# Kernel tuning notes

Measured on AMD Instinct MI355X. Metric: run time of the kernel, lower is better.

The kernel has to match this reference:

```python
import jax, jax.numpy as jnp
import numpy as np

N, E, D, H = 50000, 600000, 128, 256
EPS_DENOM = 1e-7   # epsilon added to sigmoid-edge denominator in the torch code
EPS_NORM = 1e-5    # InstanceNorm1d default eps


def _fcnn(x, Wa, ba, Wb, bb):
    # FCNN: Linear -> ReLU -> Linear
    return jax.nn.relu(x @ Wa + ba) @ Wb + bb


def setup_inputs() -> dict:
    key = jax.random.key(0)
    ks = jax.random.split(key, 16)
    inp = {
        "node_features": jax.random.normal(ks[0], (1, N, D), jnp.float32),
        "edge_index": jax.random.randint(ks[1], (1, 2, E), 0, N, dtype=jnp.int64)
        if jax.config.jax_enable_x64 else jax.random.randint(ks[1], (1, 2, E), 0, N, dtype=jnp.int32),
        "edge_features": jax.random.normal(ks[2], (1, E, D), jnp.float32),
        "global_features": jax.random.normal(ks[3], (1, 1, D), jnp.float32),
    }
    # three FCNNs: fc1 (D->H), fc2 (H->D), Kaiming-uniform-ish init scale 1/sqrt(fan_in)
    names = ["W1a", "b1a", "W1b", "b1b", "W2a", "b2a", "W2b", "b2b", "W3a", "b3a", "W3b", "b3b"]
    shapes = [(D, H), (H,), (H, D), (D,)] * 3
    fans = [D, D, H, H] * 3
    for k, (nm, sh, fan) in zip(ks[4:], zip(names, shapes, fans)):
        bound = 1.0 / np.sqrt(fan)
        inp[nm] = jax.random.uniform(k, sh, jnp.float32, -bound, bound)
    return inp


def reference(node_features, edge_index, edge_features, global_features,
              W1a, b1a, W1b, b1b, W2a, b2a, W2b, b2b, W3a, b3a, W3b, b3b):
    x = node_features[0]                      # [N, D]
    src = edge_index[0, 0]                    # [E]
    dst = edge_index[0, 1]                    # [E]
    s = jax.nn.sigmoid(edge_features[0])      # [E, D]

    # denominator: eps + sum of sigmoid(edge_feat) over all edges incident to node i
    denom = (EPS_DENOM
             + jax.ops.segment_sum(s, src, num_segments=N)
             + jax.ops.segment_sum(s, dst, num_segments=N))   # [N, D]

    h1 = _fcnn(x, W1a, b1a, W1b, b1b)                          # [N, D] self term
    h2 = _fcnn(x, W2a, b2a, W2b, b2b)                          # [N, D] neighbor term
    g3 = _fcnn(global_features[0, 0], W3a, b3a, W3b, b3b)      # [D]    global term

    # sum over incident edges of sigmoid(e) * FCNN_two(x_neighbor), then / denom
    agg = (jax.ops.segment_sum(s * h2[dst], src, num_segments=N)
           + jax.ops.segment_sum(s * h2[src], dst, num_segments=N))  # [N, D]

    inter = h1 + agg / denom + g3                              # [N, D]

    # InstanceNorm1d on a (1, D) vector: normalize over the feature dim (no affine)
    mu = jnp.mean(inter, axis=-1, keepdims=True)
    var = jnp.var(inter, axis=-1, keepdims=True)
    normed = (inter - mu) / jnp.sqrt(var + EPS_NORM)
    # dropout(p=0.1) treated as identity (inference mode)

    out = x + jax.nn.relu(normed)                              # residual update
    return out[None]                                           # [1, N, D]
```

## Files before the change

kernel.cpp:

```cpp
#include <hip/hip_runtime.h>
#include <math.h>

#define DD 128
#define HH 256

typedef __attribute__((ext_vector_type(8))) short bf16x8;
typedef __attribute__((ext_vector_type(4))) float f32x4;
typedef __attribute__((ext_vector_type(2))) float f32x2;
typedef unsigned short u16;
typedef unsigned int u32;
typedef unsigned char u8;

__device__ __forceinline__ float bf2f(u16 u) {
  union { u32 i; float f; } v; v.i = ((u32)u) << 16; return v.f;
}
__device__ __forceinline__ u16 f2bf(float f) {
  union { u32 i; float f; } v; v.f = f;
  u32 r = v.i + 0x7FFFu + ((v.i >> 16) & 1u);
  return (u16)(r >> 16);
}

#define GA_T 512
#define GA_C 512
__global__ __launch_bounds__(256) void mergeA(
    const float* __restrict__ W1a, const float* __restrict__ W1b,
    const float* __restrict__ W2a, const float* __restrict__ W2b,
    u16* __restrict__ o1, u16* __restrict__ o2,
    u16* __restrict__ o3, u16* __restrict__ o4,
    const float* __restrict__ gf,
    const float* __restrict__ W3a, const float* __restrict__ b3a,
    const float* __restrict__ W3b, const float* __restrict__ b3b,
    float* __restrict__ g3out,
    const int* __restrict__ eix, u32* __restrict__ deg, int twoE) {
  const int b = blockIdx.x;
  if (b < GA_T) {
    int idx = b * 256 + threadIdx.x;
    int m = idx >> 15;
    int r = idx & 32767;
    const float* in; u16* out; int K, Nc;
    if (m == 0)      { in = W1a; out = o1; K = DD; Nc = HH; }
    else if (m == 1) { in = W1b; out = o2; K = HH; Nc = DD; }
    else if (m == 2) { in = W2a; out = o3; K = DD; Nc = HH; }
    else             { in = W2b; out = o4; K = HH; Nc = DD; }
    int k = r / Nc, n = r % Nc;
    out[n * K + k] = f2bf(in[r]);
  } else if (b == GA_T) {
    __shared__ float gs[DD];
    __shared__ float hs[HH];
    int t = threadIdx.x;
    if (t < DD) gs[t] = gf[t];
    __syncthreads();
    float acc = b3a[t];
    for (int k = 0; k < DD; ++k) acc = fmaf(gs[k], W3a[k * HH + t], acc);
    hs[t] = acc > 0.f ? acc : 0.f;
    __syncthreads();
    if (t < DD) {
      float o = b3b[t];
      for (int j = 0; j < HH; ++j) o = fmaf(hs[j], W3b[j * DD + t], o);
      g3out[t] = o;
    }
  } else {
    int t = (b - GA_T - 1) * 256 + threadIdx.x;
    const int stride = GA_C * 256;
    for (; t < twoE; t += stride) atomicAdd(&deg[eix[t]], 1u);
  }
}

__global__ __launch_bounds__(1024) void scan_kernel(const u32* __restrict__ deg,
    u32* __restrict__ rowstart, u32* __restrict__ cursor, int N) {
  __shared__ u32 wsum[16];
  const int t = threadIdx.x;
  const int w = t >> 6, lane = t & 63;
  const int span = ((N + 1023) & ~1023) >> 4;
  const int b = w * span;
  const int e = min(b + span, N);

  u32 s = 0;
  for (int i = b + lane; i < e; i += 64) s += deg[i];
#pragma unroll
  for (int off = 32; off; off >>= 1) s += __shfl_xor(s, off);
  if (lane == 0) wsum[w] = s;
  __syncthreads();

  u32 carry = 0;
  for (int i = 0; i < w; ++i) carry += wsum[i];

  for (int i0 = b; i0 < e; i0 += 64) {
    int i = i0 + lane;
    u32 v = (i < e) ? deg[i] : 0u;
    u32 inc = v;
#pragma unroll
    for (int off = 1; off < 64; off <<= 1) {
      u32 u2 = __shfl_up(inc, off);
      if (lane >= off) inc += u2;
    }
    u32 excl = carry + inc - v;
    if (i < e) { rowstart[i] = excl; cursor[i] = excl; }
    carry += __shfl(inc, 63);
  }
  if (w == 15 && lane == 63) rowstart[N] = carry;
}

__global__ __launch_bounds__(256) void gemm_l1(const float* __restrict__ x,
    const u16* __restrict__ w1aT, const float* __restrict__ b1a,
    const u16* __restrict__ w2aT, const float* __restrict__ b2a,
    u16* __restrict__ hid, int M) {
  const int wave = (blockIdx.x * 256 + threadIdx.x) >> 6;
  const int lane = threadIdx.x & 63;
  const int totalWaves = (gridDim.x * 256) >> 6;
  const int nc = wave & 7;
  const int mw = wave >> 3;
  const int mStride = totalWaves >> 3;
  const int which = nc >> 2;
  const int c0 = (nc & 3) * 64;
  const u16* wT = which ? w2aT : w1aT;
  const float* bs = which ? b2a : b1a;
  const int l15 = lane & 15, l4 = lane >> 4;

  bf16x8 bfrag[4][4];
  float bcol[4];
#pragma unroll
  for (int t = 0; t < 4; ++t) {
    const int col = c0 + t * 16 + l15;
    const u16* bb = wT + (size_t)col * DD + l4 * 8;
#pragma unroll
    for (int kb = 0; kb < 4; ++kb) bfrag[kb][t] = *(const bf16x8*)(bb + kb * 32);
    bcol[t] = bs[col];
  }

  const int mTiles = (M + 15) >> 4;
  for (int mt = mw; mt < mTiles; mt += mStride) {
    const int m0 = mt << 4;
    int rowA = m0 + l15; if (rowA >= M) rowA = M - 1;
    const float* xr = x + (size_t)rowA * DD + l4 * 8;
    bf16x8 ax[4];
#pragma unroll
    for (int kb = 0; kb < 4; ++kb) {
      f32x4 a = *(const f32x4*)(xr + kb * 32);
      f32x4 b = *(const f32x4*)(xr + kb * 32 + 4);
      bf16x8 v;
      v[0] = (short)f2bf(a.x); v[1] = (short)f2bf(a.y);
      v[2] = (short)f2bf(a.z); v[3] = (short)f2bf(a.w);
      v[4] = (short)f2bf(b.x); v[5] = (short)f2bf(b.y);
      v[6] = (short)f2bf(b.z); v[7] = (short)f2bf(b.w);
      ax[kb] = v;
    }
    f32x4 acc[4] = {{0,0,0,0},{0,0,0,0},{0,0,0,0},{0,0,0,0}};
#pragma unroll
    for (int kb = 0; kb < 4; ++kb)
#pragma unroll
      for (int t = 0; t < 4; ++t)
        acc[t] = __builtin_amdgcn_mfma_f32_16x16x32_bf16(ax[kb], bfrag[kb][t], acc[t], 0, 0, 0);
#pragma unroll
    for (int t = 0; t < 4; ++t)
#pragma unroll
      for (int r = 0; r < 4; ++r) {
        const int row = m0 + l4 * 4 + r;
        float v = acc[t][r] + bcol[t];
        v = v > 0.f ? v : 0.f;
        if (row < M) hid[(size_t)row * 512 + which * 256 + c0 + t * 16 + l15] = f2bf(v);
      }
  }
}

__global__ __launch_bounds__(256) void gemm_l2(const u16* __restrict__ hid,
    const u16* __restrict__ w1bT, const float* __restrict__ b1b,
    const u16* __restrict__ w2bT, const float* __restrict__ b2b,
    u16* __restrict__ h1, u16* __restrict__ h2, int M) {
  const int wave = (blockIdx.x * 256 + threadIdx.x) >> 6;
  const int lane = threadIdx.x & 63;
  const int totalWaves = (gridDim.x * 256) >> 6;
  const int nc = wave & 3;
  const int mw = wave >> 2;
  const int mStride = totalWaves >> 2;
  const int which = nc >> 1;
  const int c0 = (nc & 1) * 64;
  const u16* wT = which ? w2bT : w1bT;
  const float* bs = which ? b2b : b1b;
  u16* Dst = which ? h2 : h1;
  const int l15 = lane & 15, l4 = lane >> 4;

  bf16x8 bfrag[8][4];
  float bcol[4];
#pragma unroll
  for (int t = 0; t < 4; ++t) {
    const int col = c0 + t * 16 + l15;
    const u16* bb = wT + (size_t)col * HH + l4 * 8;
#pragma unroll
    for (int kb = 0; kb < 8; ++kb) bfrag[kb][t] = *(const bf16x8*)(bb + kb * 32);
    bcol[t] = bs[col];
  }

  const int mTiles = (M + 15) >> 4;
  for (int mt = mw; mt < mTiles; mt += mStride) {
    const int m0 = mt << 4;
    int rowA = m0 + l15; if (rowA >= M) rowA = M - 1;
    const u16* arow = hid + (size_t)rowA * 512 + which * 256 + l4 * 8;
    f32x4 acc[4] = {{0,0,0,0},{0,0,0,0},{0,0,0,0},{0,0,0,0}};
#pragma unroll
    for (int kb = 0; kb < 8; ++kb) {
      bf16x8 afrag = *(const bf16x8*)(arow + kb * 32);
#pragma unroll
      for (int t = 0; t < 4; ++t)
        acc[t] = __builtin_amdgcn_mfma_f32_16x16x32_bf16(afrag, bfrag[kb][t], acc[t], 0, 0, 0);
    }
#pragma unroll
    for (int t = 0; t < 4; ++t)
#pragma unroll
      for (int r = 0; r < 4; ++r) {
        const int row = m0 + l4 * 4 + r;
        if (row < M) Dst[(size_t)row * DD + c0 + t * 16 + l15] = f2bf(acc[t][r] + bcol[t]);
      }
  }
}

#define SS_SIG  4096
#define SS_SCAT 2048
#define SS_CONV 256
__global__ __launch_bounds__(256) void mergeSS2(
    const float* __restrict__ ef, uint2* __restrict__ s8, int n8,
    const int* __restrict__ eix, u32* __restrict__ cursor,
    uint2* __restrict__ adj, int E,
    const u16* __restrict__ h2b, u32* __restrict__ h28, int n4) {
  const int b = blockIdx.x;
  if (b < SS_SIG) {
    int i = b * 256 + threadIdx.x;
    const int stride = SS_SIG * 256;
    for (; i < n8; i += stride) {
      const f32x4 a = __builtin_nontemporal_load(((const f32x4*)ef) + i * 2);
      const f32x4 bb = __builtin_nontemporal_load(((const f32x4*)ef) + i * 2 + 1);
      float s0 = 1.f / (1.f + __expf(-a.x));
      float s1 = 1.f / (1.f + __expf(-a.y));
      float s2 = 1.f / (1.f + __expf(-a.z));
      float s3 = 1.f / (1.f + __expf(-a.w));
      float s4 = 1.f / (1.f + __expf(-bb.x));
      float s5 = 1.f / (1.f + __expf(-bb.y));
      float s6 = 1.f / (1.f + __expf(-bb.z));
      float s7 = 1.f / (1.f + __expf(-bb.w));
      u32 w0 = (u32)__builtin_amdgcn_cvt_pk_fp8_f32(s0, s1, 0, false);
      w0 = (u32)__builtin_amdgcn_cvt_pk_fp8_f32(s2, s3, (int)w0, true);
      u32 w1 = (u32)__builtin_amdgcn_cvt_pk_fp8_f32(s4, s5, 0, false);
      w1 = (u32)__builtin_amdgcn_cvt_pk_fp8_f32(s6, s7, (int)w1, true);
      s8[i] = make_uint2(w0, w1);
    }
  } else if (b < SS_SIG + SS_SCAT) {
    int t = (b - SS_SIG) * 256 + threadIdx.x;
    const int stride = SS_SCAT * 256;
    const int twoE = 2 * E;
    for (; t < twoE; t += stride) {
      int node, eid, other;
      if (t < E) { node = eix[t]; eid = t;     other = eix[t + E]; }
      else       { node = eix[t]; eid = t - E; other = eix[t - E]; }
      u32 pos = atomicAdd(&cursor[node], 1u);
      adj[pos] = make_uint2((u32)eid, (u32)other);
    }
  } else {
    int i = (b - SS_SIG - SS_SCAT) * 256 + threadIdx.x;
    const int stride = SS_CONV * 256;
    for (; i < n4; i += stride) {
      uint2 hv = ((const uint2*)h2b)[i];
      float f0 = bf2f((u16)(hv.x & 0xffffu));
      float f1 = bf2f((u16)(hv.x >> 16));
      float f2 = bf2f((u16)(hv.y & 0xffffu));
      float f3 = bf2f((u16)(hv.y >> 16));
      u32 w = (u32)__builtin_amdgcn_cvt_pk_fp8_f32(f0, f1, 0, false);
      w = (u32)__builtin_amdgcn_cvt_pk_fp8_f32(f2, f3, (int)w, true);
      h28[i] = w;
    }
  }
}

__global__ __launch_bounds__(256) void gather_fp8(const float* __restrict__ x,
    const u16* __restrict__ h1, const u8* __restrict__ h28,
    const u8* __restrict__ s8, const uint2* __restrict__ adj,
    const u32* __restrict__ rowstart, const float* __restrict__ g3,
    float* __restrict__ out, int N) {
  int row0 = (blockIdx.x * 256 + threadIdx.x) >> 6;
  if (row0 >= N) return;
  const int row = __builtin_amdgcn_readfirstlane(row0);
  const int lane = threadIdx.x & 63;
  const int d0 = lane * 2;

  const u32 beg = rowstart[row];
  const u32 end = rowstart[row + 1];

  float dx = 0.f, dy = 0.f, ax = 0.f, ay = 0.f;
  u32 j = beg;
  for (; j + 8 <= end; j += 8) {
    uint2 e[8];
    u32 sv[8], hv[8];
#pragma unroll
    for (int q = 0; q < 8; ++q) e[q] = adj[j + q];
#pragma unroll
    for (int q = 0; q < 8; ++q) {
      sv[q] = *(const u16*)(s8  + (size_t)e[q].x * DD + d0);
      hv[q] = *(const u16*)(h28 + (size_t)e[q].y * DD + d0);
    }
#pragma unroll
    for (int q = 0; q < 8; ++q) {
      f32x2 sf = __builtin_amdgcn_cvt_pk_f32_fp8((int)sv[q], false);
      f32x2 hf = __builtin_amdgcn_cvt_pk_f32_fp8((int)hv[q], false);
      dx += sf.x; dy += sf.y;
      ax = fmaf(sf.x, hf.x, ax);
      ay = fmaf(sf.y, hf.y, ay);
    }
  }
  for (; j < end; ++j) {
    uint2 en = adj[j];
    u32 sv = *(const u16*)(s8  + (size_t)en.x * DD + d0);
    u32 hv = *(const u16*)(h28 + (size_t)en.y * DD + d0);
    f32x2 sf = __builtin_amdgcn_cvt_pk_f32_fp8((int)sv, false);
    f32x2 hf = __builtin_amdgcn_cvt_pk_f32_fp8((int)hv, false);
    dx += sf.x; dy += sf.y;
    ax = fmaf(sf.x, hf.x, ax);
    ay = fmaf(sf.y, hf.y, ay);
  }

  const size_t base = (size_t)row * DD + d0;
  f32x2 xv = __builtin_nontemporal_load((const f32x2*)(x + base));
  u32 h1u = __builtin_nontemporal_load((const u32*)(h1 + base));
  f32x2 gv = *(const f32x2*)(g3 + d0);

  float i0 = bf2f((u16)(h1u & 0xffffu)) + ax / (dx + 1e-7f) + gv.x;
  float i1 = bf2f((u16)(h1u >> 16)) + ay / (dy + 1e-7f) + gv.y;

  float s = i0 + i1;
  float q = i0 * i0 + i1 * i1;
#pragma unroll
  for (int off = 32; off; off >>= 1) {
    s += __shfl_xor(s, off);
    q += __shfl_xor(q, off);
  }
  float mean = s * (1.f / 128.f);
  float var = q * (1.f / 128.f) - mean * mean;
  float rstd = rsqrtf(var + 1e-5f);
  float n0v = (i0 - mean) * rstd;
  float n1v = (i1 - mean) * rstd;
  f32x2 ov;
  ov.x = xv.x + (n0v > 0.f ? n0v : 0.f);
  ov.y = xv.y + (n1v > 0.f ? n1v : 0.f);
  __builtin_nontemporal_store(ov, (f32x2*)(out + base));
}

extern "C" void kernel_launch(void* const* d_in, const int* in_sizes, int n_in,
                              void* d_out, int out_size, void* d_ws, size_t ws_size,
                              hipStream_t stream) {
  const float* x   = (const float*)d_in[0];
  const int*   eix = (const int*)d_in[1];
  const float* ef  = (const float*)d_in[2];
  const float* gf  = (const float*)d_in[3];
  const float* W1a = (const float*)d_in[4];
  const float* b1a = (const float*)d_in[5];
  const float* W1b = (const float*)d_in[6];
  const float* b1b = (const float*)d_in[7];
  const float* W2a = (const float*)d_in[8];
  const float* b2a = (const float*)d_in[9];
  const float* W2b = (const float*)d_in[10];
  const float* b2b = (const float*)d_in[11];
  const float* W3a = (const float*)d_in[12];
  const float* b3a = (const float*)d_in[13];
  const float* W3b = (const float*)d_in[14];
  const float* b3b = (const float*)d_in[15];

  const int N = in_sizes[0] / DD;
  const int E = in_sizes[2] / DD;

  char* p = (char*)d_ws;
  auto take = [&](size_t bytes) -> char* {
    char* r = p;
    p += (bytes + 255) & ~(size_t)255;
    return r;
  };
  u16* w1aT  = (u16*)take((size_t)DD * HH * 2);
  u16* w1bT  = (u16*)take((size_t)DD * HH * 2);
  u16* w2aT  = (u16*)take((size_t)DD * HH * 2);
  u16* w2bT  = (u16*)take((size_t)DD * HH * 2);
  u16* hidb  = (u16*)take((size_t)N * 512 * 2);
  u16* h1b   = (u16*)take((size_t)N * DD * 2);
  u16* h2b   = (u16*)take((size_t)N * DD * 2);
  u32* deg   = (u32*)take((size_t)N * 4);
  u32* rowst = (u32*)take((size_t)(N + 1) * 4);
  u32* curs  = (u32*)take((size_t)N * 4);
  float* g3  = (float*)take((size_t)DD * 4);
  uint2* adj = (uint2*)take((size_t)2 * E * 8);
  u8* s8     = (u8*)take((size_t)E * DD);
  u8* h28    = (u8*)take((size_t)N * DD);

  hipMemsetAsync(deg, 0, (size_t)N * 4, stream);

  mergeA<<<GA_T + 1 + GA_C, 256, 0, stream>>>(W1a, W1b, W2a, W2b,
                                              w1aT, w1bT, w2aT, w2bT,
                                              gf, W3a, b3a, W3b, b3b, g3,
                                              eix, deg, 2 * E);
  scan_kernel<<<1, 1024, 0, stream>>>(deg, rowst, curs, N);

  gemm_l1<<<2048, 256, 0, stream>>>(x, w1aT, b1a, w2aT, b2a, hidb, N);
  gemm_l2<<<2048, 256, 0, stream>>>(hidb, w1bT, b1b, w2bT, b2b, h1b, h2b, N);

  mergeSS2<<<SS_SIG + SS_SCAT + SS_CONV, 256, 0, stream>>>(
      ef, (uint2*)s8, E * DD / 8,
      eix, curs, adj, E,
      h2b, (u32*)h28, N * DD / 4);

  gather_fp8<<<(N + 3) / 4, 256, 0, stream>>>(x, h1b, h28, s8, adj, rowst, g3,
                                              (float*)d_out, N);
}
```

Measured before the change: 386.1 us.

## Emit fp8 h2 directly from gemm_l2 and fuse sigmoid with adjacency scatter per edge

gemm_l2 now converts the neighbor-term output straight to fp8 in its epilogue. That removes the bf16 h2 buffer and the separate conversion pass. The merged sigmoid/scatter/convert kernel is replaced by a per-edge kernel: one wave handles one edge's 128 sigmoid values, and two lanes do the CSR atomic inserts for that edge. The new kernel loads only 8 bytes per lane and issues single-byte fp8 stores from the GEMM epilogue, so memory access may be less efficient. It also launches many more blocks.

```diff
diff --git a/kernel.cpp b/kernel.cpp
--- a/kernel.cpp
+++ b/kernel.cpp
@@ -166,7 +166,7 @@
 __global__ __launch_bounds__(256) void gemm_l2(const u16* __restrict__ hid,
     const u16* __restrict__ w1bT, const float* __restrict__ b1b,
     const u16* __restrict__ w2bT, const float* __restrict__ b2b,
-    u16* __restrict__ h1, u16* __restrict__ h2, int M) {
+    u16* __restrict__ h1, u8* __restrict__ h28, int M) {
   const int wave = (blockIdx.x * 256 + threadIdx.x) >> 6;
   const int lane = threadIdx.x & 63;
   const int totalWaves = (gridDim.x * 256) >> 6;
@@ -177,7 +177,6 @@
   const int c0 = (nc & 1) * 64;
   const u16* wT = which ? w2bT : w1bT;
   const float* bs = which ? b2b : b1b;
-  u16* Dst = which ? h2 : h1;
   const int l15 = lane & 15, l4 = lane >> 4;
 
   bf16x8 bfrag[8][4];
@@ -209,64 +208,37 @@
 #pragma unroll
       for (int r = 0; r < 4; ++r) {
         const int row = m0 + l4 * 4 + r;
-        if (row < M) Dst[(size_t)row * DD + c0 + t * 16 + l15] = f2bf(acc[t][r] + bcol[t]);
+        if (row >= M) continue;
+        float v = acc[t][r] + bcol[t];
+        const int col = c0 + t * 16 + l15;
+        if (which) {
+          u32 w = (u32)__builtin_amdgcn_cvt_pk_fp8_f32(v, v, 0, false);
+          h28[(size_t)row * DD + col] = (u8)(w & 0xffu);
+        } else {
+          h1[(size_t)row * DD + col] = f2bf(v);
+        }
       }
   }
 }
 
-#define SS_SIG  4096
-#define SS_SCAT 2048
-#define SS_CONV 256
-__global__ __launch_bounds__(256) void mergeSS2(
-    const float* __restrict__ ef, uint2* __restrict__ s8, int n8,
-    const int* __restrict__ eix, u32* __restrict__ cursor,
-    uint2* __restrict__ adj, int E,
-    const u16* __restrict__ h2b, u32* __restrict__ h28, int n4) {
-  const int b = blockIdx.x;
-  if (b < SS_SIG) {
-    int i = b * 256 + threadIdx.x;
-    const int stride = SS_SIG * 256;
-    for (; i < n8; i += stride) {
-      const f32x4 a = __builtin_nontemporal_load(((const f32x4*)ef) + i * 2);
-      const f32x4 bb = __builtin_nontemporal_load(((const f32x4*)ef) + i * 2 + 1);
-      float s0 = 1.f / (1.f + __expf(-a.x));
-      float s1 = 1.f / (1.f + __expf(-a.y));
-      float s2 = 1.f / (1.f + __expf(-a.z));
-      float s3 = 1.f / (1.f + __expf(-a.w));
-      float s4 = 1.f / (1.f + __expf(-bb.x));
-      float s5 = 1.f / (1.f + __expf(-bb.y));
-      float s6 = 1.f / (1.f + __expf(-bb.z));
-      float s7 = 1.f / (1.f + __expf(-bb.w));
-      u32 w0 = (u32)__builtin_amdgcn_cvt_pk_fp8_f32(s0, s1, 0, false);
-      w0 = (u32)__builtin_amdgcn_cvt_pk_fp8_f32(s2, s3, (int)w0, true);
-      u32 w1 = (u32)__builtin_amdgcn_cvt_pk_fp8_f32(s4, s5, 0, false);
-      w1 = (u32)__builtin_amdgcn_cvt_pk_fp8_f32(s6, s7, (int)w1, true);
-      s8[i] = make_uint2(w0, w1);
-    }
-  } else if (b < SS_SIG + SS_SCAT) {
-    int t = (b - SS_SIG) * 256 + threadIdx.x;
-    const int stride = SS_SCAT * 256;
-    const int twoE = 2 * E;
-    for (; t < twoE; t += stride) {
-      int node, eid, other;
-      if (t < E) { node = eix[t]; eid = t;     other = eix[t + E]; }
-      else       { node = eix[t]; eid = t - E; other = eix[t - E]; }
-      u32 pos = atomicAdd(&cursor[node], 1u);
-      adj[pos] = make_uint2((u32)eid, (u32)other);
-    }
-  } else {
-    int i = (b - SS_SIG - SS_SCAT) * 256 + threadIdx.x;
-    const int stride = SS_CONV * 256;
-    for (; i < n4; i += stride) {
-      uint2 hv = ((const uint2*)h2b)[i];
-      float f0 = bf2f((u16)(hv.x & 0xffffu));
-      float f1 = bf2f((u16)(hv.x >> 16));
-      float f2 = bf2f((u16)(hv.y & 0xffffu));
-      float f3 = bf2f((u16)(hv.y >> 16));
-      u32 w = (u32)__builtin_amdgcn_cvt_pk_fp8_f32(f0, f1, 0, false);
-      w = (u32)__builtin_amdgcn_cvt_pk_fp8_f32(f2, f3, (int)w, true);
-      h28[i] = w;
-    }
+__global__ __launch_bounds__(256) void sig_scat(const float* __restrict__ ef,
+    u8* __restrict__ s8, const int* __restrict__ eix, u32* __restrict__ cursor,
+    uint2* __restrict__ adj, int E) {
+  const int e = (blockIdx.x * 256 + threadIdx.x) >> 6;
+  if (e >= E) return;
+  const int lane = threadIdx.x & 63;
+
+  f32x2 v = __builtin_nontemporal_load((const f32x2*)(ef + (size_t)e * DD + lane * 2));
+  float s0 = 1.f / (1.f + __expf(-v.x));
+  float s1 = 1.f / (1.f + __expf(-v.y));
+  u32 w = (u32)__builtin_amdgcn_cvt_pk_fp8_f32(s0, s1, 0, false);
+  *(u16*)(s8 + (size_t)e * DD + lane * 2) = (u16)w;
+
+  if (lane < 2) {
+    const int node  = eix[e + lane * E];
+    const int other = eix[e + (1 - lane) * E];
+    u32 pos = atomicAdd(&cursor[node], 1u);
+    adj[pos] = make_uint2((u32)e, (u32)other);
   }
 }
 
@@ -377,7 +349,6 @@
   u16* w2bT  = (u16*)take((size_t)DD * HH * 2);
   u16* hidb  = (u16*)take((size_t)N * 512 * 2);
   u16* h1b   = (u16*)take((size_t)N * DD * 2);
-  u16* h2b   = (u16*)take((size_t)N * DD * 2);
   u32* deg   = (u32*)take((size_t)N * 4);
   u32* rowst = (u32*)take((size_t)(N + 1) * 4);
   u32* curs  = (u32*)take((size_t)N * 4);
@@ -395,12 +366,9 @@
   scan_kernel<<<1, 1024, 0, stream>>>(deg, rowst, curs, N);
 
   gemm_l1<<<2048, 256, 0, stream>>>(x, w1aT, b1a, w2aT, b2a, hidb, N);
-  gemm_l2<<<2048, 256, 0, stream>>>(hidb, w1bT, b1b, w2bT, b2b, h1b, h2b, N);
-
-  mergeSS2<<<SS_SIG + SS_SCAT + SS_CONV, 256, 0, stream>>>(
-      ef, (uint2*)s8, E * DD / 8,
-      eix, curs, adj, E,
-      h2b, (u32*)h28, N * DD / 4);
+  gemm_l2<<<2048, 256, 0, stream>>>(hidb, w1bT, b1b, w2bT, b2b, h1b, h28, N);
+
+  sig_scat<<<(E + 3) / 4, 256, 0, stream>>>(ef, s8, eix, curs, adj, E);
 
   gather_fp8<<<(N + 3) / 4, 256, 0, stream>>>(x, h1b, h28, s8, adj, rowst, g3,
                                               (float*)d_out, N);
```

Result: slower. 420.5 us (+8.9%).

## Record atomic slot positions in degree pass and fuse fp8 conversion into GEMM epilogue

Applied to the files above, without the earlier changes.

The degree-counting pass now saves the per-edge slot returned by its atomicAdd, so the CSR scatter computes each position as rowstart plus the saved slot instead of issuing a second round of atomics on a cursor array. The h2 output of the second GEMM is written directly as fp8, which removes the bf16 h2 buffer and the separate conversion pass. The trade-off is an extra 2E-entry posrec array written and read, plus byte-wide scattered stores in the GEMM epilogue. Adjacency order within a node can still vary between runs, as it did before.

```diff
diff --git a/kernel.cpp b/kernel.cpp
--- a/kernel.cpp
+++ b/kernel.cpp
@@ -31,7 +31,8 @@
     const float* __restrict__ W3a, const float* __restrict__ b3a,
     const float* __restrict__ W3b, const float* __restrict__ b3b,
     float* __restrict__ g3out,
-    const int* __restrict__ eix, u32* __restrict__ deg, int twoE) {
+    const int* __restrict__ eix, u32* __restrict__ deg,
+    u32* __restrict__ posrec, int twoE) {
   const int b = blockIdx.x;
   if (b < GA_T) {
     int idx = b * 256 + threadIdx.x;
@@ -62,12 +63,12 @@
   } else {
     int t = (b - GA_T - 1) * 256 + threadIdx.x;
     const int stride = GA_C * 256;
-    for (; t < twoE; t += stride) atomicAdd(&deg[eix[t]], 1u);
+    for (; t < twoE; t += stride) posrec[t] = atomicAdd(&deg[eix[t]], 1u);
   }
 }
 
 __global__ __launch_bounds__(1024) void scan_kernel(const u32* __restrict__ deg,
-    u32* __restrict__ rowstart, u32* __restrict__ cursor, int N) {
+    u32* __restrict__ rowstart, int N) {
   __shared__ u32 wsum[16];
   const int t = threadIdx.x;
   const int w = t >> 6, lane = t & 63;
@@ -95,7 +96,7 @@
       if (lane >= off) inc += u2;
     }
     u32 excl = carry + inc - v;
-    if (i < e) { rowstart[i] = excl; cursor[i] = excl; }
+    if (i < e) rowstart[i] = excl;
     carry += __shfl(inc, 63);
   }
   if (w == 15 && lane == 63) rowstart[N] = carry;
@@ -166,7 +167,7 @@
 __global__ __launch_bounds__(256) void gemm_l2(const u16* __restrict__ hid,
     const u16* __restrict__ w1bT, const float* __restrict__ b1b,
     const u16* __restrict__ w2bT, const float* __restrict__ b2b,
-    u16* __restrict__ h1, u16* __restrict__ h2, int M) {
+    u16* __restrict__ h1, u8* __restrict__ h28, int M) {
   const int wave = (blockIdx.x * 256 + threadIdx.x) >> 6;
   const int lane = threadIdx.x & 63;
   const int totalWaves = (gridDim.x * 256) >> 6;
@@ -177,7 +178,6 @@
   const int c0 = (nc & 1) * 64;
   const u16* wT = which ? w2bT : w1bT;
   const float* bs = which ? b2b : b1b;
-  u16* Dst = which ? h2 : h1;
   const int l15 = lane & 15, l4 = lane >> 4;
 
   bf16x8 bfrag[8][4];
@@ -209,19 +209,25 @@
 #pragma unroll
       for (int r = 0; r < 4; ++r) {
         const int row = m0 + l4 * 4 + r;
-        if (row < M) Dst[(size_t)row * DD + c0 + t * 16 + l15] = f2bf(acc[t][r] + bcol[t]);
+        if (row >= M) continue;
+        float v = acc[t][r] + bcol[t];
+        const int col = c0 + t * 16 + l15;
+        if (which) {
+          u32 w = (u32)__builtin_amdgcn_cvt_pk_fp8_f32(v, v, 0, false);
+          h28[(size_t)row * DD + col] = (u8)(w & 0xffu);
+        } else {
+          h1[(size_t)row * DD + col] = f2bf(v);
+        }
       }
   }
 }
 
 #define SS_SIG  4096
-#define SS_SCAT 2048
-#define SS_CONV 256
-__global__ __launch_bounds__(256) void mergeSS2(
+#define SS_SCAT 1024
+__global__ __launch_bounds__(256) void mergeSS3(
     const float* __restrict__ ef, uint2* __restrict__ s8, int n8,
-    const int* __restrict__ eix, u32* __restrict__ cursor,
-    uint2* __restrict__ adj, int E,
-    const u16* __restrict__ h2b, u32* __restrict__ h28, int n4) {
+    const int* __restrict__ eix, const u32* __restrict__ rowstart,
+    const u32* __restrict__ posrec, uint2* __restrict__ adj, int E) {
   const int b = blockIdx.x;
   if (b < SS_SIG) {
     int i = b * 256 + threadIdx.x;
@@ -243,7 +249,7 @@
       w1 = (u32)__builtin_amdgcn_cvt_pk_fp8_f32(s6, s7, (int)w1, true);
       s8[i] = make_uint2(w0, w1);
     }
-  } else if (b < SS_SIG + SS_SCAT) {
+  } else {
     int t = (b - SS_SIG) * 256 + threadIdx.x;
     const int stride = SS_SCAT * 256;
     const int twoE = 2 * E;
@@ -251,21 +257,8 @@
       int node, eid, other;
       if (t < E) { node = eix[t]; eid = t;     other = eix[t + E]; }
       else       { node = eix[t]; eid = t - E; other = eix[t - E]; }
-      u32 pos = atomicAdd(&cursor[node], 1u);
+      u32 pos = rowstart[node] + posrec[t];
       adj[pos] = make_uint2((u32)eid, (u32)other);
-    }
-  } else {
-    int i = (b - SS_SIG - SS_SCAT) * 256 + threadIdx.x;
-    const int stride = SS_CONV * 256;
-    for (; i < n4; i += stride) {
-      uint2 hv = ((const uint2*)h2b)[i];
-      float f0 = bf2f((u16)(hv.x & 0xffffu));
-      float f1 = bf2f((u16)(hv.x >> 16));
-      float f2 = bf2f((u16)(hv.y & 0xffffu));
-      float f3 = bf2f((u16)(hv.y >> 16));
-      u32 w = (u32)__builtin_amdgcn_cvt_pk_fp8_f32(f0, f1, 0, false);
-      w = (u32)__builtin_amdgcn_cvt_pk_fp8_f32(f2, f3, (int)w, true);
-      h28[i] = w;
     }
   }
 }
@@ -371,36 +364,33 @@
     p += (bytes + 255) & ~(size_t)255;
     return r;
   };
-  u16* w1aT  = (u16*)take((size_t)DD * HH * 2);
-  u16* w1bT  = (u16*)take((size_t)DD * HH * 2);
-  u16* w2aT  = (u16*)take((size_t)DD * HH * 2);
-  u16* w2bT  = (u16*)take((size_t)DD * HH * 2);
-  u16* hidb  = (u16*)take((size_t)N * 512 * 2);
-  u16* h1b   = (u16*)take((size_t)N * DD * 2);
-  u16* h2b   = (u16*)take((size_t)N * DD * 2);
-  u32* deg   = (u32*)take((size_t)N * 4);
-  u32* rowst = (u32*)take((size_t)(N + 1) * 4);
-  u32* curs  = (u32*)take((size_t)N * 4);
-  float* g3  = (float*)take((size_t)DD * 4);
-  uint2* adj = (uint2*)take((size_t)2 * E * 8);
-  u8* s8     = (u8*)take((size_t)E * DD);
-  u8* h28    = (u8*)take((size_t)N * DD);
+  u16* w1aT   = (u16*)take((size_t)DD * HH * 2);
+  u16* w1bT   = (u16*)take((size_t)DD * HH * 2);
+  u16* w2aT   = (u16*)take((size_t)DD * HH * 2);
+  u16* w2bT   = (u16*)take((size_t)DD * HH * 2);
+  u16* hidb   = (u16*)take((size_t)N * 512 * 2);
+  u16* h1b    = (u16*)take((size_t)N * DD * 2);
+  u32* deg    = (u32*)take((size_t)N * 4);
+  u32* rowst  = (u32*)take((size_t)(N + 1) * 4);
+  u32* posrec = (u32*)take((size_t)2 * E * 4);
+  float* g3   = (float*)take((size_t)DD * 4);
+  uint2* adj  = (uint2*)take((size_t)2 * E * 8);
+  u8* s8      = (u8*)take((size_t)E * DD);
+  u8* h28     = (u8*)take((size_t)N * DD);
 
   hipMemsetAsync(deg, 0, (size_t)N * 4, stream);
 
   mergeA<<<GA_T + 1 + GA_C, 256, 0, stream>>>(W1a, W1b, W2a, W2b,
                                               w1aT, w1bT, w2aT, w2bT,
                                               gf, W3a, b3a, W3b, b3b, g3,
-                                              eix, deg, 2 * E);
-  scan_kernel<<<1, 1024, 0, stream>>>(deg, rowst, curs, N);
+                                              eix, deg, posrec, 2 * E);
+  scan_kernel<<<1, 1024, 0, stream>>>(deg, rowst, N);
 
   gemm_l1<<<2048, 256, 0, stream>>>(x, w1aT, b1a, w2aT, b2a, hidb, N);
-  gemm_l2<<<2048, 256, 0, stream>>>(hidb, w1bT, b1b, w2bT, b2b, h1b, h2b, N);
-
-  mergeSS2<<<SS_SIG + SS_SCAT + SS_CONV, 256, 0, stream>>>(
-      ef, (uint2*)s8, E * DD / 8,
-      eix, curs, adj, E,
-      h2b, (u32*)h28, N * DD / 4);
+  gemm_l2<<<2048, 256, 0, stream>>>(hidb, w1bT, b1b, w2bT, b2b, h1b, h28, N);
+
+  mergeSS3<<<SS_SIG + SS_SCAT, 256, 0, stream>>>(ef, (uint2*)s8, E * DD / 8,
+                                                 eix, rowst, posrec, adj, E);
 
   gather_fp8<<<(N + 3) / 4, 256, 0, stream>>>(x, h1b, h28, s8, adj, rowst, g3,
                                               (float*)d_out, N);
```

After: 345.6 us. 10.5% less time.
